# Optimization experiments

Hardware: AMD Instinct MI355X
Metric: run time of the kernel (lower is better)

The kernel has to match this reference:

```python
import jax, jax.numpy as jnp
import numpy as np

PROPOSAL_COUNT = 1000
NMS_THRESHOLD = 0.7
PRE_NMS_LIMIT = 6000
RPN_BBOX_STD_DEV = np.array([0.1, 0.1, 0.2, 0.2], dtype=np.float32)
B, N = 4, 261888


def setup_inputs() -> dict:
    key = jax.random.key(0)
    k1, k2, k3, k4, k5, k6 = jax.random.split(key, 6)
    logits = jax.random.normal(k1, (B, N, 2), dtype=jnp.float32)
    rpn_probs = jax.nn.softmax(logits, axis=-1)
    rpn_deltas = jax.random.normal(k2, (B, N, 4), dtype=jnp.float32) * 0.1
    # anchors as valid normalized boxes (y1,x1,y2,x2)
    cy = jax.random.uniform(k3, (B, N), dtype=jnp.float32)
    cx = jax.random.uniform(k4, (B, N), dtype=jnp.float32)
    h = jax.random.uniform(k5, (B, N), dtype=jnp.float32) * 0.2 + 0.02
    w = jax.random.uniform(k6, (B, N), dtype=jnp.float32) * 0.2 + 0.02
    anchors = jnp.stack([cy - 0.5 * h, cx - 0.5 * w, cy + 0.5 * h, cx + 0.5 * w], axis=-1)
    return {"rpn_probs": rpn_probs, "rpn_deltas": rpn_deltas, "anchors": anchors}


def apply_box_deltas(boxes, deltas):
    # boxes, deltas: [K, 4]
    h = boxes[:, 2] - boxes[:, 0]
    w = boxes[:, 3] - boxes[:, 1]
    cy = boxes[:, 0] + 0.5 * h + deltas[:, 0] * h
    cx = boxes[:, 1] + 0.5 * w + deltas[:, 1] * w
    h = h * jnp.exp(deltas[:, 2])
    w = w * jnp.exp(deltas[:, 3])
    y1 = cy - 0.5 * h
    x1 = cx - 0.5 * w
    return jnp.stack([y1, x1, y1 + h, x1 + w], axis=1)


def _iou_matrix(boxes):
    # boxes: [K, 4] -> IoU [K, K]
    y1, x1, y2, x2 = jnp.split(boxes, 4, axis=1)  # each [K,1]
    area = (y2 - y1) * (x2 - x1)
    ih = jnp.maximum(jnp.minimum(y2, y2.T) - jnp.maximum(y1, y1.T), 0.0)
    iw = jnp.maximum(jnp.minimum(x2, x2.T) - jnp.maximum(x1, x1.T), 0.0)
    inter = ih * iw
    return inter / (area + area.T - inter + 1e-8)


def nms_single(boxes, scores):
    # boxes: [K,4] already sorted by descending score; greedy NMS like tf.image.non_max_suppression
    K = boxes.shape[0]
    iou = _iou_matrix(jax.lax.stop_gradient(boxes))

    def body(i, suppressed):
        keep_i = jnp.logical_not(suppressed[i])
        new = jnp.where(keep_i, jnp.logical_or(suppressed, iou[i] > NMS_THRESHOLD), suppressed)
        return new.at[i].set(suppressed[i])

    suppressed = jax.lax.fori_loop(0, K, body, jnp.zeros((K,), dtype=bool))
    keep = jnp.logical_not(suppressed)
    # stable: kept indices first (already score-sorted), then take top proposal_count
    order = jnp.argsort(jnp.where(keep, jnp.arange(K), K))
    sel = order[:PROPOSAL_COUNT]
    valid = jnp.arange(PROPOSAL_COUNT) < jnp.sum(keep)
    return boxes[sel] * valid[:, None].astype(boxes.dtype)  # zero-pad like tf.pad


def reference(rpn_probs, rpn_deltas, anchors):
    scores = rpn_probs[:, :, 1]                              # [B, N] fg scores
    deltas = rpn_deltas * RPN_BBOX_STD_DEV.reshape(1, 1, 4)  # [B, N, 4]
    k = min(PRE_NMS_LIMIT, anchors.shape[1])
    top_scores, ix = jax.lax.top_k(scores, k)                # sorted descending
    deltas_k = jnp.take_along_axis(deltas, ix[:, :, None], axis=1)   # [B, k, 4]
    anchors_k = jnp.take_along_axis(anchors, ix[:, :, None], axis=1)  # [B, k, 4]
    boxes = jax.vmap(apply_box_deltas)(anchors_k, deltas_k)
    boxes = jnp.clip(boxes, 0.0, 1.0)                        # window [0,0,1,1]
    return jax.vmap(nms_single)(boxes, top_scores)           # [B, proposal_count, 4]
```

## Files before the change

### kernel.cpp

```cpp
#include <hip/hip_runtime.h>

typedef unsigned int u32;
typedef unsigned long long u64;

#define BB 4
#define NN 261888
#define KSEL 6000
#define CAP 8192
#define PC 1000
#define NMS_THR 0.7f
#define NW 94
#define NWP 96
#define NR (NW*64)
#define COLSPLIT 6

#define HB 31
#define CHUNK_H (NN/HB)
#define HITER (CHUNK_H/256)
#define CB 93
#define CHUNK_C (NN/CB)
#define CITER (CHUNK_C/256)

#define CS 4
#define CPS (CAP/CS)

#define HIST1_OFF 0
#define HIST2_OFF (BB*2048)
#define SEL_OFF   (BB*2048*2)
#define CNT_OFF   (BB*2048*2 + BB*4)
#define RANK_OFF  (BB*2048*2 + BB*4 + BB*32)
#define ZERO_WORDS (BB*2048*2 + BB*4 + BB*32 + BB*CAP)

__global__ void k_zero(u32* ws) {
    int i = blockIdx.x * 256 + threadIdx.x;
    if (i < ZERO_WORDS) ws[i] = 0u;
}

__global__ void k_hist1(const float2* __restrict__ probs2, u32* __restrict__ hist1) {
    __shared__ u32 lh[2048];
    int b = blockIdx.y;
    size_t base = (size_t)b * NN + (size_t)blockIdx.x * CHUNK_H;
    for (int j = threadIdx.x; j < 2048; j += 256) lh[j] = 0u;
    __syncthreads();
    #pragma unroll 4
    for (int it = 0; it < HITER; ++it) {
        float2 p = probs2[base + it * 256 + threadIdx.x];
        atomicAdd(&lh[__float_as_uint(p.y) >> 21], 1u);
    }
    __syncthreads();
    for (int j = threadIdx.x; j < 2048; j += 256) {
        u32 c = lh[j];
        if (c) atomicAdd(&hist1[b * 2048 + j], c);
    }
}

__global__ void k_sel1(const u32* __restrict__ hist1, u32* __restrict__ sel) {
    __shared__ u32 gsum[256];
    __shared__ u32 lh[2048];
    int b = blockIdx.x;
    int t = threadIdx.x;
    u32 s = 0;
    #pragma unroll
    for (int j = 0; j < 8; ++j) {
        u32 v = hist1[b * 2048 + 2047 - (t * 8 + j)];
        lh[t * 8 + j] = v;
        s += v;
    }
    gsum[t] = s;
    __syncthreads();
    if (t == 0) {
        u32 cum = 0;
        for (int g = 0; g < 256; ++g) {
            if (cum + gsum[g] >= (u32)KSEL) {
                for (int j = 0; j < 8; ++j) {
                    u32 c = lh[g * 8 + j];
                    if (cum + c >= (u32)KSEL) {
                        sel[b * 4 + 0] = (u32)(2047 - (g * 8 + j));
                        sel[b * 4 + 1] = cum;
                        break;
                    }
                    cum += c;
                }
                break;
            }
            cum += gsum[g];
        }
    }
}

__global__ void k_hist2(const float2* __restrict__ probs2, const u32* __restrict__ sel,
                        u32* __restrict__ hist2) {
    int b = blockIdx.y;
    u32 b1 = sel[b * 4 + 0];
    size_t base = (size_t)b * NN + (size_t)blockIdx.x * CHUNK_H;
    #pragma unroll 4
    for (int it = 0; it < HITER; ++it) {
        float2 p = probs2[base + it * 256 + threadIdx.x];
        u32 key = __float_as_uint(p.y);
        if ((key >> 21) == b1) atomicAdd(&hist2[b * 2048 + ((key >> 10) & 2047u)], 1u);
    }
}

__global__ void k_sel2(const u32* __restrict__ hist2, u32* __restrict__ sel) {
    __shared__ u32 gsum[256];
    __shared__ u32 lh[2048];
    int b = blockIdx.x;
    int t = threadIdx.x;
    u32 s = 0;
    #pragma unroll
    for (int j = 0; j < 8; ++j) {
        u32 v = hist2[b * 2048 + 2047 - (t * 8 + j)];
        lh[t * 8 + j] = v;
        s += v;
    }
    gsum[t] = s;
    __syncthreads();
    if (t == 0) {
        u32 cum = sel[b * 4 + 1];
        u32 b1 = sel[b * 4 + 0];
        for (int g = 0; g < 256; ++g) {
            if (cum + gsum[g] >= (u32)KSEL) {
                for (int j = 0; j < 8; ++j) {
                    cum += lh[g * 8 + j];
                    if (cum >= (u32)KSEL) {
                        sel[b * 4 + 2] = (b1 << 11) | (u32)(2047 - (g * 8 + j));
                        break;
                    }
                }
                break;
            }
            cum += gsum[g];
        }
    }
}

__global__ void k_compact(const float2* __restrict__ probs2, const u32* __restrict__ sel,
                          u32* __restrict__ candCount, u64* __restrict__ cand) {
    __shared__ u32 wsum[4];
    __shared__ u32 blkBase;
    int b = blockIdx.y;
    int tid = threadIdx.x;
    int wave = tid >> 6, lane = tid & 63;
    u32 base = (u32)blockIdx.x * CHUNK_C;
    u32 thr = sel[b * 4 + 2];

    u32 keys[CITER];
    u32 cnt = 0;
    #pragma unroll
    for (int it = 0; it < CITER; ++it) {
        float2 p = probs2[(size_t)b * NN + base + it * 256 + tid];
        u32 key = __float_as_uint(p.y);
        keys[it] = key;
        cnt += ((key >> 10) >= thr) ? 1u : 0u;
    }
    #pragma unroll
    for (int off = 32; off; off >>= 1) cnt += __shfl_down(cnt, off);
    if (lane == 0) wsum[wave] = cnt;
    __syncthreads();
    if (tid == 0) {
        u32 w0 = wsum[0], w1 = wsum[1], w2 = wsum[2], w3 = wsum[3];
        u32 tot = w0 + w1 + w2 + w3;
        wsum[0] = 0; wsum[1] = w0; wsum[2] = w0 + w1; wsum[3] = w0 + w1 + w2;
        blkBase = tot ? atomicAdd(&candCount[b * 32], tot) : 0u;
    }
    __syncthreads();
    u32 run = blkBase + wsum[wave];
    u64* cb = cand + (size_t)b * CAP;
    #pragma unroll
    for (int it = 0; it < CITER; ++it) {
        u32 key = keys[it];
        bool pred = (key >> 10) >= thr;
        u64 m = __ballot(pred);
        if (pred) {
            u32 pos = run + (u32)__popcll(m & ((1ull << lane) - 1ull));
            u32 gi = base + it * 256 + tid;
            if (pos < CAP) cb[pos] = ((u64)key << 32) | (u32)(~gi);
        }
        run += (u32)__popcll(m);
    }
}

__global__ __launch_bounds__(512) void k_rank(const u64* __restrict__ cand,
                                              const u32* __restrict__ candCount,
                                              u32* __restrict__ rankArr) {
    __shared__ u64 keys[CPS];
    int b = blockIdx.z;
    int c0 = blockIdx.y * CPS;
    int tid = threadIdx.x;
    int cnt = (int)candCount[b * 32];
    if (cnt > CAP) cnt = CAP;
    const u64* cb = cand + (size_t)b * CAP;
    for (int j = tid; j < CPS; j += 512)
        keys[j] = (c0 + j < cnt) ? cb[c0 + j] : 0ull;
    __syncthreads();
    int r = blockIdx.x * 512 + tid;
    if (r >= cnt) return;
    u64 my = cb[r];
    u32 rank = 0;
    for (int j = 0; j < CPS; j += 16) {
        #pragma unroll
        for (int u = 0; u < 16; ++u)
            rank += (keys[j + u] > my) ? 1u : 0u;
    }
    if (rank) atomicAdd(&rankArr[b * CAP + r], rank);
}

__global__ void k_scatterdecode(const u64* __restrict__ cand, const u32* __restrict__ candCount,
                                const u32* __restrict__ rankArr,
                                const float4* __restrict__ anchors,
                                const float4* __restrict__ deltas,
                                float4* __restrict__ boxes) {
    int b = blockIdx.y;
    int p = blockIdx.x * 256 + threadIdx.x;
    int cnt = (int)candCount[b * 32];
    if (cnt > CAP) cnt = CAP;
    if (p >= cnt) return;
    u32 rank = rankArr[b * CAP + p];
    if (rank >= KSEL) return;
    u64 sk = cand[(size_t)b * CAP + p];
    u32 idx = ~(u32)(sk & 0xFFFFFFFFull);
    if (idx >= NN) idx = NN - 1;
    float4 a = anchors[(size_t)b * NN + idx];
    float4 d = deltas[(size_t)b * NN + idx];
    float dy = __fmul_rn(d.x, 0.1f);
    float dx = __fmul_rn(d.y, 0.1f);
    float dh = __fmul_rn(d.z, 0.2f);
    float dw = __fmul_rn(d.w, 0.2f);
    float h  = __fsub_rn(a.z, a.x);
    float w  = __fsub_rn(a.w, a.y);
    float cy = __fadd_rn(__fadd_rn(a.x, __fmul_rn(0.5f, h)), __fmul_rn(dy, h));
    float cx = __fadd_rn(__fadd_rn(a.y, __fmul_rn(0.5f, w)), __fmul_rn(dx, w));
    float h2 = __fmul_rn(h, expf(dh));
    float w2 = __fmul_rn(w, expf(dw));
    float y1 = __fsub_rn(cy, __fmul_rn(0.5f, h2));
    float x1 = __fsub_rn(cx, __fmul_rn(0.5f, w2));
    float y2 = __fadd_rn(y1, h2);
    float x2 = __fadd_rn(x1, w2);
    y1 = fminf(fmaxf(y1, 0.0f), 1.0f);
    x1 = fminf(fmaxf(x1, 0.0f), 1.0f);
    y2 = fminf(fmaxf(y2, 0.0f), 1.0f);
    x2 = fminf(fmaxf(x2, 0.0f), 1.0f);
    float4 out;
    out.x = y1; out.y = x1; out.z = y2; out.w = x2;
    boxes[(size_t)b * KSEL + rank] = out;
}

__global__ void k_sortgather(const u64* __restrict__ cand, const u32* __restrict__ candCount,
                             const float4* __restrict__ anchors, const float4* __restrict__ deltas,
                             float4* __restrict__ boxes) {
    __shared__ u64 s[CAP];
    int b = blockIdx.x;
    int tid = threadIdx.x;
    u32 cnt = candCount[b * 32];
    if (cnt > CAP) cnt = CAP;
    for (int j = tid; j < CAP; j += 1024)
        s[j] = (j < (int)cnt) ? cand[(size_t)b * CAP + j] : 0ull;
    __syncthreads();
    for (int k = 2; k <= CAP; k <<= 1) {
        for (int j = k >> 1; j > 0; j >>= 1) {
            for (int idx = tid; idx < CAP; idx += 1024) {
                int l = idx ^ j;
                if (l > idx) {
                    u64 a = s[idx], c = s[l];
                    bool dir = ((idx & k) == 0);
                    if ((a < c) == dir) { s[idx] = c; s[l] = a; }
                }
            }
            __syncthreads();
        }
    }
    for (int t = tid; t < KSEL; t += 1024) {
        u64 sk = s[t];
        u32 idx = ~(u32)(sk & 0xFFFFFFFFull);
        float4 a = anchors[(size_t)b * NN + idx];
        float4 d = deltas[(size_t)b * NN + idx];
        float dy = __fmul_rn(d.x, 0.1f);
        float dx = __fmul_rn(d.y, 0.1f);
        float dh = __fmul_rn(d.z, 0.2f);
        float dw = __fmul_rn(d.w, 0.2f);
        float h  = __fsub_rn(a.z, a.x);
        float w  = __fsub_rn(a.w, a.y);
        float cy = __fadd_rn(__fadd_rn(a.x, __fmul_rn(0.5f, h)), __fmul_rn(dy, h));
        float cx = __fadd_rn(__fadd_rn(a.y, __fmul_rn(0.5f, w)), __fmul_rn(dx, w));
        float h2 = __fmul_rn(h, expf(dh));
        float w2 = __fmul_rn(w, expf(dw));
        float y1 = __fsub_rn(cy, __fmul_rn(0.5f, h2));
        float x1 = __fsub_rn(cx, __fmul_rn(0.5f, w2));
        float y2 = __fadd_rn(y1, h2);
        float x2 = __fadd_rn(x1, w2);
        y1 = fminf(fmaxf(y1, 0.0f), 1.0f);
        x1 = fminf(fmaxf(x1, 0.0f), 1.0f);
        y2 = fminf(fmaxf(y2, 0.0f), 1.0f);
        x2 = fminf(fmaxf(x2, 0.0f), 1.0f);
        float4 out;
        out.x = y1; out.y = x1; out.z = y2; out.w = x2;
        boxes[(size_t)b * KSEL + t] = out;
    }
}

__global__ __launch_bounds__(256) void k_iou(const float4* __restrict__ boxes,
                                             u64* __restrict__ mask) {
    __shared__ float4 colBox[4][64];
    __shared__ float  colArea[4][64];
    int b = blockIdx.z;
    int rblk = blockIdx.x;
    int r0 = rblk * 64;
    int tid = threadIdx.x;
    int wave = tid >> 6, lane = tid & 63;
    const float4* B4 = boxes + (size_t)b * KSEL;

    int r = r0 + lane;
    float4 rb;
    if (r < KSEL) rb = B4[r];
    else { rb.x = 2.0f; rb.y = 2.0f; rb.z = 3.0f; rb.w = 3.0f; }
    float ra = __fmul_rn(__fsub_rn(rb.z, rb.x), __fsub_rn(rb.w, rb.y));

    const double M0 = 0.5 * ((double)__uint_as_float(0x3F333333u)
                           + (double)__uint_as_float(0x3F333334u));
    u64* Mb = mask + (size_t)b * NR * NWP;

    for (int jw = rblk + blockIdx.y * 4 + wave; jw < NW; jw += 4 * COLSPLIT) {
        int j = jw * 64 + lane;
        float4 cbx;
        if (j < KSEL) cbx = B4[j];
        else { cbx.x = 2.0f; cbx.y = 2.0f; cbx.z = 3.0f; cbx.w = 3.0f; }
        colBox[wave][lane] = cbx;
        colArea[wave][lane] = __fmul_rn(__fsub_rn(cbx.z, cbx.x), __fsub_rn(cbx.w, cbx.y));
        asm volatile("" ::: "memory");

        u64 word = 0ull;
        #pragma unroll
        for (int c = 0; c < 64; ++c) {
            float4 cb = colBox[wave][c];
            float ca = colArea[wave][c];
            float ih = fmaxf(__fsub_rn(fminf(rb.z, cb.z), fmaxf(rb.x, cb.x)), 0.0f);
            float iw = fmaxf(__fsub_rn(fminf(rb.w, cb.w), fmaxf(rb.y, cb.y)), 0.0f);
            float inter = __fmul_rn(ih, iw);
            float denom = __fadd_rn(__fsub_rn(__fadd_rn(ra, ca), inter), 1e-8f);
            bool pred = ((double)inter >= M0 * (double)denom);
            word |= ((u64)pred) << c;
        }
        Mb[(size_t)(r0 + lane) * NWP + jw] = word;
        asm volatile("" ::: "memory");
    }
}

__device__ __forceinline__ u64 readlane64(u64 v, int lane) {
    u32 lo = (u32)__builtin_amdgcn_readlane((int)(u32)v, lane);
    u32 hi = (u32)__builtin_amdgcn_readlane((int)(u32)(v >> 32), lane);
    return ((u64)hi << 32) | (u64)lo;
}
__device__ __forceinline__ u64 rfl64(u64 v) {
    u32 lo = (u32)__builtin_amdgcn_readfirstlane((int)(u32)v);
    u32 hi = (u32)__builtin_amdgcn_readfirstlane((int)(u32)(v >> 32));
    return ((u64)hi << 32) | (u64)lo;
}
__device__ __forceinline__ void barrier_lds_only() {
    asm volatile("s_waitcnt lgkmcnt(0)" ::: "memory");
    __builtin_amdgcn_s_barrier();
    asm volatile("" ::: "memory");
}

__global__ __launch_bounds__(1024) void k_reduce(const u64* __restrict__ mask,
                                                 const float4* __restrict__ boxes,
                                                 float* __restrict__ outp) {
    __shared__ u64 pub[16];
    __shared__ u64 kbLDS;
    __shared__ u32 kLDS;
    __shared__ u32 keptIdx[PC];
    int b = blockIdx.x;
    int tid = threadIdx.x;
    int wv = tid >> 6, lane = tid & 63;
    const u64* M = mask + (size_t)b * NR * NWP;
    const float4* B4 = boxes + (size_t)b * KSEL;
    int lp = lane < 46 ? lane : 46;
    u64 rwA = 0ull, rwB = 0ull;
    int k = 0, kprev = 0;
    bool done = false;

    if (tid < 16) pub[tid] = 0ull;

    ulonglong2 bufA[4], bufB[4], bufC[4];
    u64 dgA, dgB, dgC;

#define LOADG(BUF, DG, gg) do {                                               \
    int gl_ = (gg); if (gl_ > NW - 1) gl_ = NW - 1;                           \
    _Pragma("unroll")                                                         \
    for (int r_ = 0; r_ < 4; ++r_)                                            \
        BUF[r_] = *(const ulonglong2*)(M + (size_t)(gl_ * 64 + wv * 4 + r_) * NWP + 2 * lp); \
    DG = M[(size_t)(gl_ * 64 + lane) * NWP + gl_];                            \
} while (0)

#define BODY(gg, CUR, DGC, NXT, DGN) do {                                     \
    const int gb_ = (gg);                                                     \
    LOADG(NXT, DGN, gb_ + 2);                                                 \
    if (wv == 0) {                                                            \
        u64 rem = pub[0] | pub[1] | pub[2] | pub[3]                           \
                | pub[4] | pub[5] | pub[6] | pub[7]                           \
                | pub[8] | pub[9] | pub[10] | pub[11]                         \
                | pub[12] | pub[13] | pub[14] | pub[15];                      \
        rem = rfl64(rem);                                                     \
        int remaining = KSEL - gb_ * 64;                                      \
        u64 valid = (remaining >= 64) ? ~0ull : ((1ull << remaining) - 1ull); \
        u64 todo = ~rem & valid;                                              \
        u64 kb0 = 0ull;                                                       \
        int k0 = k;                                                           \
        while (todo && k0 < PC) {                                             \
            u64 t_ = todo;                                                    \
            int i0 = (int)__builtin_ctzll(t_); t_ &= t_ - 1;                  \
            bool v1 = t_ != 0ull;                                             \
            int i1 = v1 ? (int)__builtin_ctzll(t_) : i0; t_ &= t_ - 1;        \
            bool v2 = t_ != 0ull;                                             \
            int i2 = v2 ? (int)__builtin_ctzll(t_) : i0; t_ &= t_ - 1;        \
            bool v3 = t_ != 0ull;                                             \
            int i3 = v3 ? (int)__builtin_ctzll(t_) : i0;                      \
            u64 m0 = __ballot(((DGC >> i0) & 1ull) != 0ull);                  \
            u64 m1 = __ballot(((DGC >> i1) & 1ull) != 0ull);                  \
            u64 m2 = __ballot(((DGC >> i2) & 1ull) != 0ull);                  \
            u64 m3 = __ballot(((DGC >> i3) & 1ull) != 0ull);                  \
            u64 kept_ = 1ull << i0; ++k0;                                     \
            u64 sup_ = m0;                                                    \
            if (v1 && k0 < PC && !((sup_ >> i1) & 1ull)) {                    \
                kept_ |= 1ull << i1; ++k0; sup_ |= m1;                        \
            }                                                                 \
            if (v2 && k0 < PC && !((sup_ >> i2) & 1ull)) {                    \
                kept_ |= 1ull << i2; ++k0; sup_ |= m2;                        \
            }                                                                 \
            if (v3 && k0 < PC && !((sup_ >> i3) & 1ull)) {                    \
                kept_ |= 1ull << i3; ++k0; sup_ |= m3;                        \
            }                                                                 \
            kb0 |= kept_;                                                     \
            todo &= ~(sup_ | kept_);                                          \
            if (k0 >= PC) break;                                              \
        }                                                                     \
        if ((kb0 >> lane) & 1ull) {                                           \
            int rank = kprev + (int)__popcll(kb0 & ((1ull << lane) - 1ull));  \
            keptIdx[rank] = (u32)(gb_ * 64 + lane);                           \
        }                                                                     \
        kprev = k0;                                                           \
        if (lane == 0) { kbLDS = kb0; kLDS = (u32)k0; }                       \
    }                                                                         \
    barrier_lds_only();                                                       \
    u64 kb_ = kbLDS;                                                          \
    k = (int)kLDS;                                                            \
    _Pragma("unroll")                                                         \
    for (int r_ = 0; r_ < 4; ++r_)                                            \
        if ((kb_ >> (wv * 4 + r_)) & 1ull) { rwA |= CUR[r_].x; rwB |= CUR[r_].y; } \
    if (k >= PC || gb_ == NW - 1) { done = true; }                            \
    else {                                                                    \
        int nw_ = gb_ + 1;                                                    \
        u64 wpub = (nw_ & 1) ? readlane64(rwB, nw_ >> 1)                      \
                             : readlane64(rwA, nw_ >> 1);                     \
        if (lane == 0) pub[wv] = wpub;                                        \
        barrier_lds_only();                                                   \
    }                                                                         \
} while (0)

    LOADG(bufA, dgA, 0);
    LOADG(bufB, dgB, 1);
    __syncthreads();

    for (int g = 0; g < NW && !done; g += 3) {
        BODY(g, bufA, dgA, bufC, dgC);
        if (done || g + 1 >= NW) break;
        BODY(g + 1, bufB, dgB, bufA, dgA);
        if (done || g + 2 >= NW) break;
        BODY(g + 2, bufC, dgC, bufB, dgB);
    }
    __syncthreads();

    float4* O = (float4*)outp + (size_t)b * PC;
    for (int t = tid; t < PC; t += 1024) {
        float4 v; v.x = 0.0f; v.y = 0.0f; v.z = 0.0f; v.w = 0.0f;
        if (t < k) v = B4[keptIdx[t]];
        O[t] = v;
    }
#undef LOADG
#undef BODY
}

__global__ void k_nms(const float4* __restrict__ boxes, float* __restrict__ outp) {
    __shared__ float4 chunk[512];
    __shared__ float4 keptBox[PC];
    __shared__ float  keptArea[PC];
    __shared__ u32    flag[2];
    int b = blockIdx.x;
    int tid = threadIdx.x;
    const float4* B4 = boxes + (size_t)b * KSEL;

    if (tid < 2) flag[tid] = 0u;
    for (int j = tid; j < 512; j += 256) chunk[j] = B4[j];
    __syncthreads();

    int kc = 0;
    for (int i = 0; i < KSEL && kc < PC; ++i) {
        int ci = i & 511;
        if (ci == 0 && i != 0) {
            for (int j = tid; j < 512 && (i + j) < KSEL; j += 256) chunk[j] = B4[i + j];
            __syncthreads();
        }
        float4 cb = chunk[ci];
        float careaV = __fmul_rn(__fsub_rn(cb.z, cb.x), __fsub_rn(cb.w, cb.y));
        bool sup = false;
        for (int t = tid; t < kc; t += 256) {
            float4 kb2 = keptBox[t];
            float ih = fmaxf(__fsub_rn(fminf(cb.z, kb2.z), fmaxf(cb.x, kb2.x)), 0.0f);
            float iw = fmaxf(__fsub_rn(fminf(cb.w, kb2.w), fmaxf(cb.y, kb2.y)), 0.0f);
            float inter = __fmul_rn(ih, iw);
            float denom = __fadd_rn(__fsub_rn(__fadd_rn(careaV, keptArea[t]), inter), 1e-8f);
            if (__fdiv_rn(inter, denom) > NMS_THR) sup = true;
        }
        int p = i & 1;
        if (sup) flag[p] = 1u;
        if (tid == 0) flag[p ^ 1] = 0u;
        __syncthreads();
        if (flag[p] == 0u) {
            if (tid == 0) { keptBox[kc] = cb; keptArea[kc] = careaV; }
            kc++;
        }
        __syncthreads();
    }

    float4* out4 = (float4*)outp + (size_t)b * PC;
    for (int r = tid; r < PC; r += 256) {
        float4 v;
        if (r < kc) v = keptBox[r];
        else { v.x = 0.0f; v.y = 0.0f; v.z = 0.0f; v.w = 0.0f; }
        out4[r] = v;
    }
}

extern "C" void kernel_launch(void* const* d_in, const int* in_sizes, int n_in,
                              void* d_out, int out_size, void* d_ws, size_t ws_size,
                              hipStream_t stream) {
    const float* probs   = (const float*)d_in[0];
    const float* deltas  = (const float*)d_in[1];
    const float* anchors = (const float*)d_in[2];
    float* outp = (float*)d_out;

    u32* ws32 = (u32*)d_ws;
    u32* hist1 = ws32 + HIST1_OFF;
    u32* hist2 = ws32 + HIST2_OFF;
    u32* sel   = ws32 + SEL_OFF;
    u32* candCount = ws32 + CNT_OFF;
    u32* rankArr   = ws32 + RANK_OFF;
    u64* cand   = (u64*)(ws32 + ZERO_WORDS);
    float* boxesF = (float*)(cand + (size_t)BB * CAP);
    float4* boxes = (float4*)boxesF;
    u64* mask = (u64*)(boxesF + (size_t)BB * KSEL * 4);

    size_t needed = (size_t)ZERO_WORDS * 4 + (size_t)BB * CAP * 8
                  + (size_t)BB * KSEL * 16 + (size_t)BB * NR * NWP * 8;

    hipLaunchKernelGGL(k_zero, dim3((ZERO_WORDS + 255) / 256), dim3(256), 0, stream, ws32);
    hipLaunchKernelGGL(k_hist1, dim3(HB, BB), dim3(256), 0, stream, (const float2*)probs, hist1);
    hipLaunchKernelGGL(k_sel1, dim3(BB), dim3(256), 0, stream, hist1, sel);
    hipLaunchKernelGGL(k_hist2, dim3(HB, BB), dim3(256), 0, stream, (const float2*)probs, sel, hist2);
    hipLaunchKernelGGL(k_sel2, dim3(BB), dim3(256), 0, stream, hist2, sel);
    hipLaunchKernelGGL(k_compact, dim3(CB, BB), dim3(256), 0, stream, (const float2*)probs, sel, candCount, cand);
    if (ws_size >= needed) {
        hipLaunchKernelGGL(k_rank, dim3(CAP / 512, CS, BB), dim3(512), 0, stream, cand, candCount, rankArr);
        hipLaunchKernelGGL(k_scatterdecode, dim3(CAP / 256, BB), dim3(256), 0, stream,
                           cand, candCount, rankArr,
                           (const float4*)anchors, (const float4*)deltas, boxes);
        hipLaunchKernelGGL(k_iou, dim3(NW, COLSPLIT, BB), dim3(256), 0, stream, boxes, mask);
        hipLaunchKernelGGL(k_reduce, dim3(BB), dim3(1024), 0, stream, mask, boxes, outp);
    } else {
        hipLaunchKernelGGL(k_sortgather, dim3(BB), dim3(1024), 0, stream,
                           cand, candCount, (const float4*)anchors, (const float4*)deltas, boxes);
        hipLaunchKernelGGL(k_nms, dim3(BB), dim3(256), 0, stream, boxes, outp);
    }
}
```

Baseline: 213.6 us.

## Fuse radix-select histogram and compaction stages into one cooperative kernel

Replaces the five kernels for the two histogram passes, two threshold selections and compaction with one cooperative kernel that uses grid-wide syncs. Each block loads its chunk of scores into registers once and reuses them for both histograms and the compaction, instead of reading the probabilities three times. The second histogram now accumulates in shared memory before flushing to global atomics. It also removes the fallback sort/NMS path. The cost is grid.sync overhead, a 124-block cooperative grid with each thread holding 33 keys in registers, and idle blocks during the single-block selection phases.

```diff
diff --git a/kernel.cpp b/kernel.cpp
--- a/kernel.cpp
+++ b/kernel.cpp
@@ -1,4 +1,7 @@
 #include <hip/hip_runtime.h>
+#include <hip/hip_cooperative_groups.h>
+
+namespace cg = cooperative_groups;
 
 typedef unsigned int u32;
 typedef unsigned long long u64;
@@ -17,9 +20,6 @@
 #define HB 31
 #define CHUNK_H (NN/HB)
 #define HITER (CHUNK_H/256)
-#define CB 93
-#define CHUNK_C (NN/CB)
-#define CITER (CHUNK_C/256)
 
 #define CS 4
 #define CPS (CAP/CS)
@@ -36,123 +36,117 @@
     if (i < ZERO_WORDS) ws[i] = 0u;
 }
 
-__global__ void k_hist1(const float2* __restrict__ probs2, u32* __restrict__ hist1) {
+__global__ void k_select(const float2* __restrict__ probs2,
+                         u32* __restrict__ hist1, u32* __restrict__ hist2,
+                         u32* __restrict__ sel, u32* __restrict__ candCount,
+                         u64* __restrict__ cand) {
+    cg::grid_group grid = cg::this_grid();
     __shared__ u32 lh[2048];
-    int b = blockIdx.y;
-    size_t base = (size_t)b * NN + (size_t)blockIdx.x * CHUNK_H;
-    for (int j = threadIdx.x; j < 2048; j += 256) lh[j] = 0u;
-    __syncthreads();
-    #pragma unroll 4
-    for (int it = 0; it < HITER; ++it) {
-        float2 p = probs2[base + it * 256 + threadIdx.x];
-        atomicAdd(&lh[__float_as_uint(p.y) >> 21], 1u);
-    }
-    __syncthreads();
-    for (int j = threadIdx.x; j < 2048; j += 256) {
-        u32 c = lh[j];
-        if (c) atomicAdd(&hist1[b * 2048 + j], c);
-    }
-}
-
-__global__ void k_sel1(const u32* __restrict__ hist1, u32* __restrict__ sel) {
     __shared__ u32 gsum[256];
-    __shared__ u32 lh[2048];
-    int b = blockIdx.x;
-    int t = threadIdx.x;
-    u32 s = 0;
-    #pragma unroll
-    for (int j = 0; j < 8; ++j) {
-        u32 v = hist1[b * 2048 + 2047 - (t * 8 + j)];
-        lh[t * 8 + j] = v;
-        s += v;
-    }
-    gsum[t] = s;
-    __syncthreads();
-    if (t == 0) {
-        u32 cum = 0;
-        for (int g = 0; g < 256; ++g) {
-            if (cum + gsum[g] >= (u32)KSEL) {
-                for (int j = 0; j < 8; ++j) {
-                    u32 c = lh[g * 8 + j];
-                    if (cum + c >= (u32)KSEL) {
-                        sel[b * 4 + 0] = (u32)(2047 - (g * 8 + j));
-                        sel[b * 4 + 1] = cum;
-                        break;
-                    }
-                    cum += c;
-                }
-                break;
-            }
-            cum += gsum[g];
-        }
-    }
-}
-
-__global__ void k_hist2(const float2* __restrict__ probs2, const u32* __restrict__ sel,
-                        u32* __restrict__ hist2) {
-    int b = blockIdx.y;
-    u32 b1 = sel[b * 4 + 0];
-    size_t base = (size_t)b * NN + (size_t)blockIdx.x * CHUNK_H;
-    #pragma unroll 4
-    for (int it = 0; it < HITER; ++it) {
-        float2 p = probs2[base + it * 256 + threadIdx.x];
-        u32 key = __float_as_uint(p.y);
-        if ((key >> 21) == b1) atomicAdd(&hist2[b * 2048 + ((key >> 10) & 2047u)], 1u);
-    }
-}
-
-__global__ void k_sel2(const u32* __restrict__ hist2, u32* __restrict__ sel) {
-    __shared__ u32 gsum[256];
-    __shared__ u32 lh[2048];
-    int b = blockIdx.x;
-    int t = threadIdx.x;
-    u32 s = 0;
-    #pragma unroll
-    for (int j = 0; j < 8; ++j) {
-        u32 v = hist2[b * 2048 + 2047 - (t * 8 + j)];
-        lh[t * 8 + j] = v;
-        s += v;
-    }
-    gsum[t] = s;
-    __syncthreads();
-    if (t == 0) {
-        u32 cum = sel[b * 4 + 1];
-        u32 b1 = sel[b * 4 + 0];
-        for (int g = 0; g < 256; ++g) {
-            if (cum + gsum[g] >= (u32)KSEL) {
-                for (int j = 0; j < 8; ++j) {
-                    cum += lh[g * 8 + j];
-                    if (cum >= (u32)KSEL) {
-                        sel[b * 4 + 2] = (b1 << 11) | (u32)(2047 - (g * 8 + j));
-                        break;
-                    }
-                }
-                break;
-            }
-            cum += gsum[g];
-        }
-    }
-}
-
-__global__ void k_compact(const float2* __restrict__ probs2, const u32* __restrict__ sel,
-                          u32* __restrict__ candCount, u64* __restrict__ cand) {
     __shared__ u32 wsum[4];
     __shared__ u32 blkBase;
     int b = blockIdx.y;
     int tid = threadIdx.x;
     int wave = tid >> 6, lane = tid & 63;
-    u32 base = (u32)blockIdx.x * CHUNK_C;
+    size_t base = (size_t)b * NN + (size_t)blockIdx.x * CHUNK_H;
+
+    u32 keys[HITER];
+
+    for (int j = tid; j < 2048; j += 256) lh[j] = 0u;
+    __syncthreads();
+    #pragma unroll
+    for (int it = 0; it < HITER; ++it) {
+        float2 p = probs2[base + it * 256 + tid];
+        keys[it] = __float_as_uint(p.y);
+        atomicAdd(&lh[keys[it] >> 21], 1u);
+    }
+    __syncthreads();
+    for (int j = tid; j < 2048; j += 256) {
+        u32 c = lh[j];
+        if (c) atomicAdd(&hist1[b * 2048 + j], c);
+    }
+    grid.sync();
+
+    if (blockIdx.x == 0) {
+        u32 s = 0;
+        #pragma unroll
+        for (int j = 0; j < 8; ++j) {
+            u32 v = hist1[b * 2048 + 2047 - (tid * 8 + j)];
+            lh[tid * 8 + j] = v;
+            s += v;
+        }
+        gsum[tid] = s;
+        __syncthreads();
+        if (tid == 0) {
+            u32 cum = 0;
+            for (int g = 0; g < 256; ++g) {
+                if (cum + gsum[g] >= (u32)KSEL) {
+                    for (int j = 0; j < 8; ++j) {
+                        u32 c = lh[g * 8 + j];
+                        if (cum + c >= (u32)KSEL) {
+                            sel[b * 4 + 0] = (u32)(2047 - (g * 8 + j));
+                            sel[b * 4 + 1] = cum;
+                            break;
+                        }
+                        cum += c;
+                    }
+                    break;
+                }
+                cum += gsum[g];
+            }
+        }
+    }
+    grid.sync();
+
+    u32 b1 = sel[b * 4 + 0];
+    for (int j = tid; j < 2048; j += 256) lh[j] = 0u;
+    __syncthreads();
+    #pragma unroll
+    for (int it = 0; it < HITER; ++it) {
+        u32 key = keys[it];
+        if ((key >> 21) == b1) atomicAdd(&lh[(key >> 10) & 2047u], 1u);
+    }
+    __syncthreads();
+    for (int j = tid; j < 2048; j += 256) {
+        u32 c = lh[j];
+        if (c) atomicAdd(&hist2[b * 2048 + j], c);
+    }
+    grid.sync();
+
+    if (blockIdx.x == 0) {
+        u32 s = 0;
+        #pragma unroll
+        for (int j = 0; j < 8; ++j) {
+            u32 v = hist2[b * 2048 + 2047 - (tid * 8 + j)];
+            lh[tid * 8 + j] = v;
+            s += v;
+        }
+        gsum[tid] = s;
+        __syncthreads();
+        if (tid == 0) {
+            u32 cum = sel[b * 4 + 1];
+            for (int g = 0; g < 256; ++g) {
+                if (cum + gsum[g] >= (u32)KSEL) {
+                    for (int j = 0; j < 8; ++j) {
+                        cum += lh[g * 8 + j];
+                        if (cum >= (u32)KSEL) {
+                            sel[b * 4 + 2] = (b1 << 11) | (u32)(2047 - (g * 8 + j));
+                            break;
+                        }
+                    }
+                    break;
+                }
+                cum += gsum[g];
+            }
+        }
+    }
+    grid.sync();
+
     u32 thr = sel[b * 4 + 2];
-
-    u32 keys[CITER];
     u32 cnt = 0;
     #pragma unroll
-    for (int it = 0; it < CITER; ++it) {
-        float2 p = probs2[(size_t)b * NN + base + it * 256 + tid];
-        u32 key = __float_as_uint(p.y);
-        keys[it] = key;
-        cnt += ((key >> 10) >= thr) ? 1u : 0u;
-    }
+    for (int it = 0; it < HITER; ++it)
+        cnt += ((keys[it] >> 10) >= thr) ? 1u : 0u;
     #pragma unroll
     for (int off = 32; off; off >>= 1) cnt += __shfl_down(cnt, off);
     if (lane == 0) wsum[wave] = cnt;
@@ -166,14 +160,15 @@
     __syncthreads();
     u32 run = blkBase + wsum[wave];
     u64* cb = cand + (size_t)b * CAP;
+    u32 cbase = (u32)blockIdx.x * CHUNK_H;
     #pragma unroll
-    for (int it = 0; it < CITER; ++it) {
+    for (int it = 0; it < HITER; ++it) {
         u32 key = keys[it];
         bool pred = (key >> 10) >= thr;
         u64 m = __ballot(pred);
         if (pred) {
             u32 pos = run + (u32)__popcll(m & ((1ull << lane) - 1ull));
-            u32 gi = base + it * 256 + tid;
+            u32 gi = cbase + it * 256 + tid;
             if (pos < CAP) cb[pos] = ((u64)key << 32) | (u32)(~gi);
         }
         run += (u32)__popcll(m);
@@ -243,59 +238,6 @@
     float4 out;
     out.x = y1; out.y = x1; out.z = y2; out.w = x2;
     boxes[(size_t)b * KSEL + rank] = out;
-}
-
-__global__ void k_sortgather(const u64* __restrict__ cand, const u32* __restrict__ candCount,
-                             const float4* __restrict__ anchors, const float4* __restrict__ deltas,
-                             float4* __restrict__ boxes) {
-    __shared__ u64 s[CAP];
-    int b = blockIdx.x;
-    int tid = threadIdx.x;
-    u32 cnt = candCount[b * 32];
-    if (cnt > CAP) cnt = CAP;
-    for (int j = tid; j < CAP; j += 1024)
-        s[j] = (j < (int)cnt) ? cand[(size_t)b * CAP + j] : 0ull;
-    __syncthreads();
-    for (int k = 2; k <= CAP; k <<= 1) {
-        for (int j = k >> 1; j > 0; j >>= 1) {
-            for (int idx = tid; idx < CAP; idx += 1024) {
-                int l = idx ^ j;
-                if (l > idx) {
-                    u64 a = s[idx], c = s[l];
-                    bool dir = ((idx & k) == 0);
-                    if ((a < c) == dir) { s[idx] = c; s[l] = a; }
-                }
-            }
-            __syncthreads();
-        }
-    }
-    for (int t = tid; t < KSEL; t += 1024) {
-        u64 sk = s[t];
-        u32 idx = ~(u32)(sk & 0xFFFFFFFFull);
-        float4 a = anchors[(size_t)b * NN + idx];
-        float4 d = deltas[(size_t)b * NN + idx];
-        float dy = __fmul_rn(d.x, 0.1f);
-        float dx = __fmul_rn(d.y, 0.1f);
-        float dh = __fmul_rn(d.z, 0.2f);
-        float dw = __fmul_rn(d.w, 0.2f);
-        float h  = __fsub_rn(a.z, a.x);
-        float w  = __fsub_rn(a.w, a.y);
-        float cy = __fadd_rn(__fadd_rn(a.x, __fmul_rn(0.5f, h)), __fmul_rn(dy, h));
-        float cx = __fadd_rn(__fadd_rn(a.y, __fmul_rn(0.5f, w)), __fmul_rn(dx, w));
-        float h2 = __fmul_rn(h, expf(dh));
-        float w2 = __fmul_rn(w, expf(dw));
-        float y1 = __fsub_rn(cy, __fmul_rn(0.5f, h2));
-        float x1 = __fsub_rn(cx, __fmul_rn(0.5f, w2));
-        float y2 = __fadd_rn(y1, h2);
-        float x2 = __fadd_rn(x1, w2);
-        y1 = fminf(fmaxf(y1, 0.0f), 1.0f);
-        x1 = fminf(fmaxf(x1, 0.0f), 1.0f);
-        y2 = fminf(fmaxf(y2, 0.0f), 1.0f);
-        x2 = fminf(fmaxf(x2, 0.0f), 1.0f);
-        float4 out;
-        out.x = y1; out.y = x1; out.z = y2; out.w = x2;
-        boxes[(size_t)b * KSEL + t] = out;
-    }
 }
 
 __global__ __launch_bounds__(256) void k_iou(const float4* __restrict__ boxes,
@@ -479,57 +421,6 @@
 #undef BODY
 }
 
-__global__ void k_nms(const float4* __restrict__ boxes, float* __restrict__ outp) {
-    __shared__ float4 chunk[512];
-    __shared__ float4 keptBox[PC];
-    __shared__ float  keptArea[PC];
-    __shared__ u32    flag[2];
-    int b = blockIdx.x;
-    int tid = threadIdx.x;
-    const float4* B4 = boxes + (size_t)b * KSEL;
-
-    if (tid < 2) flag[tid] = 0u;
-    for (int j = tid; j < 512; j += 256) chunk[j] = B4[j];
-    __syncthreads();
-
-    int kc = 0;
-    for (int i = 0; i < KSEL && kc < PC; ++i) {
-        int ci = i & 511;
-        if (ci == 0 && i != 0) {
-            for (int j = tid; j < 512 && (i + j) < KSEL; j += 256) chunk[j] = B4[i + j];
-            __syncthreads();
-        }
-        float4 cb = chunk[ci];
-        float careaV = __fmul_rn(__fsub_rn(cb.z, cb.x), __fsub_rn(cb.w, cb.y));
-        bool sup = false;
-        for (int t = tid; t < kc; t += 256) {
-            float4 kb2 = keptBox[t];
-            float ih = fmaxf(__fsub_rn(fminf(cb.z, kb2.z), fmaxf(cb.x, kb2.x)), 0.0f);
-            float iw = fmaxf(__fsub_rn(fminf(cb.w, kb2.w), fmaxf(cb.y, kb2.y)), 0.0f);
-            float inter = __fmul_rn(ih, iw);
-            float denom = __fadd_rn(__fsub_rn(__fadd_rn(careaV, keptArea[t]), inter), 1e-8f);
-            if (__fdiv_rn(inter, denom) > NMS_THR) sup = true;
-        }
-        int p = i & 1;
-        if (sup) flag[p] = 1u;
-        if (tid == 0) flag[p ^ 1] = 0u;
-        __syncthreads();
-        if (flag[p] == 0u) {
-            if (tid == 0) { keptBox[kc] = cb; keptArea[kc] = careaV; }
-            kc++;
-        }
-        __syncthreads();
-    }
-
-    float4* out4 = (float4*)outp + (size_t)b * PC;
-    for (int r = tid; r < PC; r += 256) {
-        float4 v;
-        if (r < kc) v = keptBox[r];
-        else { v.x = 0.0f; v.y = 0.0f; v.z = 0.0f; v.w = 0.0f; }
-        out4[r] = v;
-    }
-}
-
 extern "C" void kernel_launch(void* const* d_in, const int* in_sizes, int n_in,
                               void* d_out, int out_size, void* d_ws, size_t ws_size,
                               hipStream_t stream) {
@@ -549,25 +440,20 @@
     float4* boxes = (float4*)boxesF;
     u64* mask = (u64*)(boxesF + (size_t)BB * KSEL * 4);
 
-    size_t needed = (size_t)ZERO_WORDS * 4 + (size_t)BB * CAP * 8
-                  + (size_t)BB * KSEL * 16 + (size_t)BB * NR * NWP * 8;
-
     hipLaunchKernelGGL(k_zero, dim3((ZERO_WORDS + 255) / 256), dim3(256), 0, stream, ws32);
-    hipLaunchKernelGGL(k_hist1, dim3(HB, BB), dim3(256), 0, stream, (const float2*)probs, hist1);
-    hipLaunchKernelGGL(k_sel1, dim3(BB), dim3(256), 0, stream, hist1, sel);
-    hipLaunchKernelGGL(k_hist2, dim3(HB, BB), dim3(256), 0, stream, (const float2*)probs, sel, hist2);
-    hipLaunchKernelGGL(k_sel2, dim3(BB), dim3(256), 0, stream, hist2, sel);
-    hipLaunchKernelGGL(k_compact, dim3(CB, BB), dim3(256), 0, stream, (const float2*)probs, sel, candCount, cand);
-    if (ws_size >= needed) {
-        hipLaunchKernelGGL(k_rank, dim3(CAP / 512, CS, BB), dim3(512), 0, stream, cand, candCount, rankArr);
-        hipLaunchKernelGGL(k_scatterdecode, dim3(CAP / 256, BB), dim3(256), 0, stream,
-                           cand, candCount, rankArr,
-                           (const float4*)anchors, (const float4*)deltas, boxes);
-        hipLaunchKernelGGL(k_iou, dim3(NW, COLSPLIT, BB), dim3(256), 0, stream, boxes, mask);
-        hipLaunchKernelGGL(k_reduce, dim3(BB), dim3(1024), 0, stream, mask, boxes, outp);
-    } else {
-        hipLaunchKernelGGL(k_sortgather, dim3(BB), dim3(1024), 0, stream,
-                           cand, candCount, (const float4*)anchors, (const float4*)deltas, boxes);
-        hipLaunchKernelGGL(k_nms, dim3(BB), dim3(256), 0, stream, boxes, outp);
-    }
-}
+
+    {
+        const float2* probs2 = (const float2*)probs;
+        void* args[] = { (void*)&probs2, (void*)&hist1, (void*)&hist2,
+                         (void*)&sel, (void*)&candCount, (void*)&cand };
+        hipLaunchCooperativeKernel((const void*)k_select, dim3(HB, BB), dim3(256),
+                                   args, 0, stream);
+    }
+
+    hipLaunchKernelGGL(k_rank, dim3(CAP / 512, CS, BB), dim3(512), 0, stream, cand, candCount, rankArr);
+    hipLaunchKernelGGL(k_scatterdecode, dim3(CAP / 256, BB), dim3(256), 0, stream,
+                       cand, candCount, rankArr,
+                       (const float4*)anchors, (const float4*)deltas, boxes);
+    hipLaunchKernelGGL(k_iou, dim3(NW, COLSPLIT, BB), dim3(256), 0, stream, boxes, mask);
+    hipLaunchKernelGGL(k_reduce, dim3(BB), dim3(1024), 0, stream, mask, boxes, outp);
+}
```

Result: slower. 253.0 us (+18.5%).
